# Kernel optimization log

Measured on AMD Instinct MI355X. Metric: run time of the kernel, lower is better.

## Reference

```python
import jax, jax.numpy as jnp
import numpy as np


def setup_inputs() -> dict:
    key = jax.random.key(0)
    kq, kk, kv = jax.random.split(key, 3)
    B, Q, K, D = 8, 2048, 2048, 1024
    return {
        "queries": jax.random.normal(kq, (B, Q, D), dtype=jnp.float32),
        "keys": jax.random.normal(kk, (B, K, D), dtype=jnp.float32),
        "values": jax.random.normal(kv, (B, K, D), dtype=jnp.float32),
    }


def reference(queries, keys, values):
    # scores: [B, Q, K] = queries @ keys^T
    scores = jnp.einsum("bqd,bkd->bqk", queries, keys)
    # NOTE: softmax over dim=1, i.e. the QUERY axis (non-standard)
    attn = jax.nn.softmax(scores, axis=1)
    # output: [B, Q, D]
    return jnp.einsum("bqk,bkd->bqd", attn, values)
```

## Files before the change

kernel.cpp:

```cpp
#include <hip/hip_runtime.h>
#include <stdint.h>

typedef _Float16 half8 __attribute__((ext_vector_type(8)));
typedef __attribute__((ext_vector_type(4))) float f32x4;
typedef __attribute__((ext_vector_type(8))) unsigned short us8;

__device__ inline unsigned short f2h(float x) {
  _Float16 h = (_Float16)x;
  return __builtin_bit_cast(unsigned short, h);
}

__device__ inline void ld16(const unsigned short* g, unsigned short* l) {
  __builtin_amdgcn_global_load_lds(
      (const __attribute__((address_space(1))) unsigned int*)g,
      (__attribute__((address_space(3))) unsigned int*)l, 16, 0, 0);
}

__global__ void k_cast16(const float* __restrict__ in, unsigned short* __restrict__ o, long n8) {
  long i = (long)blockIdx.x * blockDim.x + threadIdx.x;
  if (i >= n8) return;
  float4 a = ((const float4*)in)[i * 2];
  float4 b = ((const float4*)in)[i * 2 + 1];
  us8 h;
  h[0] = f2h(a.x); h[1] = f2h(a.y); h[2] = f2h(a.z); h[3] = f2h(a.w);
  h[4] = f2h(b.x); h[5] = f2h(b.y); h[6] = f2h(b.z); h[7] = f2h(b.w);
  *(us8*)(o + i * 8) = h;
}

__global__ void k_cast16c(const float* __restrict__ in, unsigned short* __restrict__ o,
                          int Kn, int Dn, int k0c, int Kc) {
  const long i = (long)blockIdx.x * blockDim.x + threadIdx.x;
  const long cols8 = (long)Kc * Dn / 8;
  const int b = (int)(i / cols8);
  const long j = i - (long)b * cols8;
  const float* p = in + (long)b * Kn * Dn + (long)k0c * Dn + j * 8;
  float4 a = *(const float4*)p;
  float4 c = *(const float4*)(p + 4);
  us8 h;
  h[0] = f2h(a.x); h[1] = f2h(a.y); h[2] = f2h(a.z); h[3] = f2h(a.w);
  h[4] = f2h(c.x); h[5] = f2h(c.y); h[6] = f2h(c.z); h[7] = f2h(c.w);
  *(us8*)(o + (long)b * Kc * Dn + j * 8) = h;
}

__global__ void k_transpose16(const float* __restrict__ V, unsigned short* __restrict__ VT,
                              int Kn, int Dn, int k0c, int Kc) {
  __shared__ unsigned short t[64][65];
  const int b = blockIdx.z;
  const int k0 = blockIdx.x * 64, d0 = blockIdx.y * 64;
  const int c = threadIdx.x & 63, rr = threadIdx.x >> 6;
  const float* pV = V + (long)b * Kn * Dn;
  unsigned short* pT = VT + (long)b * Dn * Kc;
#pragma unroll
  for (int i = 0; i < 16; ++i) {
    int r = rr + i * 4;
    t[r][c] = f2h(pV[(long)(k0c + k0 + r) * Dn + d0 + c]);
  }
  __syncthreads();
#pragma unroll
  for (int i = 0; i < 16; ++i) {
    int r = rr + i * 4;
    pT[(long)(d0 + r) * Kc + k0 + c] = t[c][r];
  }
}


#define SBAR() __builtin_amdgcn_s_barrier()
#define SCHED0() __builtin_amdgcn_sched_barrier(0)
#define VMC(n) do { asm volatile("s_waitcnt vmcnt(" #n ")" ::: "memory"); } while (0)

template <int STATS, int ACC>
__launch_bounds__(512, 2)
__global__ void k_gemm_bt(const unsigned short* __restrict__ A,
                          const unsigned short* __restrict__ B,
                          float* __restrict__ C, float2* __restrict__ ps,
                          int N, int Kin, long sA, long sB, long sC) {
  __shared__ unsigned short sAb[4][256 * 32];
  __shared__ unsigned short sBb[4][256 * 32];

  const int tid = threadIdx.x;
  const int lane = tid & 63, wave = tid >> 6;
  const int wr = wave >> 2, wc = wave & 3;
  const int l15 = lane & 15;

  const int nx = gridDim.x, ny = gridDim.y;
  int wg = ((int)blockIdx.z * ny + blockIdx.y) * nx + blockIdx.x;
  const int nwg = nx * ny * (int)gridDim.z;
  wg = (wg & 7) * (nwg >> 3) + (wg >> 3);
  const int tn = wg % nx, tm = (wg / nx) % ny, b = wg / (nx * ny);

  const unsigned short* pA = A + b * sA + (long)tm * 256 * Kin;
  const unsigned short* pB = B + b * sB + (long)tn * 256 * Kin;
  float* pC = C + b * sC;

  const int rlo = tid >> 2;
  const int csw = ((tid & 3) * 8) ^ (((rlo >> 1) & 3) << 3);
  const long ga = (long)rlo * Kin + csw;
  const long gh = (long)128 * Kin;

  const int ksw = ((lane >> 4) * 8) ^ (((l15 >> 1) & 3) << 3);
  const int aoff = (wr * 128 + l15) * 32 + ksw;
  const int boff = (wc * 64 + l15) * 32 + ksw;

#define STG(t, q) do { \
    ld16(pA + ga + (long)(t) * 32, &sAb[q][tid * 8]); \
    ld16(pA + ga + gh + (long)(t) * 32, &sAb[q][4096 + tid * 8]); \
    ld16(pB + ga + (long)(t) * 32, &sBb[q][tid * 8]); \
    ld16(pB + ga + gh + (long)(t) * 32, &sBb[q][4096 + tid * 8]); } while (0)

#define LDA8(q, m) (*(const half8*)&sAb[q][aoff + (m) * 512])
#define LDB8(q, n) (*(const half8*)&sBb[q][boff + (n) * 512])

  f32x4 acc[8][4];
#pragma unroll
  for (int i = 0; i < 8; ++i)
#pragma unroll
    for (int j = 0; j < 4; ++j)
#pragma unroll
      for (int r = 0; r < 4; ++r) acc[i][j][r] = 0.f;

  half8 aL[2][4], bC[2][4], aH[4];

#define READ_LO(s, q) \
  aL[s][0] = LDA8(q, 0); aL[s][1] = LDA8(q, 1); aL[s][2] = LDA8(q, 2); aL[s][3] = LDA8(q, 3); \
  bC[s][0] = LDB8(q, 0); bC[s][1] = LDB8(q, 1); bC[s][2] = LDB8(q, 2); bC[s][3] = LDB8(q, 3);

#define READ_HI(q) \
  aH[0] = LDA8(q, 4); aH[1] = LDA8(q, 5); aH[2] = LDA8(q, 6); aH[3] = LDA8(q, 7);

#define MFMA_ROW(m, a, s) \
  acc[m][0] = __builtin_amdgcn_mfma_f32_16x16x32_f16(a, bC[s][0], acc[m][0], 0, 0, 0); \
  acc[m][1] = __builtin_amdgcn_mfma_f32_16x16x32_f16(a, bC[s][1], acc[m][1], 0, 0, 0); \
  acc[m][2] = __builtin_amdgcn_mfma_f32_16x16x32_f16(a, bC[s][2], acc[m][2], 0, 0, 0); \
  acc[m][3] = __builtin_amdgcn_mfma_f32_16x16x32_f16(a, bC[s][3], acc[m][3], 0, 0, 0);

#define MFMA_LO(s) \
  __builtin_amdgcn_s_setprio(1); \
  MFMA_ROW(0, aL[s][0], s) MFMA_ROW(1, aL[s][1], s) \
  MFMA_ROW(2, aL[s][2], s) MFMA_ROW(3, aL[s][3], s) \
  __builtin_amdgcn_s_setprio(0);

#define MFMA_HI(s) \
  __builtin_amdgcn_s_setprio(1); \
  MFMA_ROW(4, aH[0], s) MFMA_ROW(5, aH[1], s) \
  MFMA_ROW(6, aH[2], s) MFMA_ROW(7, aH[3], s) \
  __builtin_amdgcn_s_setprio(0);

#define TILE_MAIN(t, s, sn) \
  READ_HI((t) & 3); \
  STG((t) + 2, ((t) + 2) & 3); \
  MFMA_LO(s) \
  VMC(4); SBAR(); SCHED0(); \
  READ_LO(sn, ((t) + 1) & 3); \
  MFMA_HI(s)

  const int nt = Kin >> 5;

  STG(0, 0);
  STG(1, 1);
  VMC(4); SBAR(); SCHED0();
  READ_LO(0, 0);

  for (int t = 0; t + 3 < nt; t += 2) {
    TILE_MAIN(t, 0, 1);
    TILE_MAIN(t + 1, 1, 0);
  }
  {
    READ_HI((nt - 2) & 3);
    MFMA_LO(0)
    VMC(0); SBAR(); SCHED0();
    READ_LO(1, (nt - 1) & 3);
    MFMA_HI(0)
    READ_HI((nt - 1) & 3);
    MFMA_LO(1)
    MFMA_HI(1)
  }

  const int crow0 = tm * 256 + wr * 128 + (lane >> 4) * 4;
  const int ccol0 = tn * 256 + wc * 64 + l15;
#pragma unroll
  for (int m = 0; m < 8; ++m)
#pragma unroll
    for (int n = 0; n < 4; ++n)
#pragma unroll
      for (int r = 0; r < 4; ++r) {
        long idx = (long)(crow0 + m * 16 + r) * N + ccol0 + n * 16;
        if constexpr (ACC) pC[idx] += acc[m][n][r];
        else pC[idx] = acc[m][n][r];
      }

  if constexpr (STATS) {
#pragma unroll
    for (int n = 0; n < 4; ++n) {
      float mx = -3.0e38f;
#pragma unroll
      for (int m = 0; m < 8; ++m)
#pragma unroll
        for (int r = 0; r < 4; ++r) mx = fmaxf(mx, acc[m][n][r]);
      mx = fmaxf(mx, __shfl_xor(mx, 16, 64));
      mx = fmaxf(mx, __shfl_xor(mx, 32, 64));
      float l = 0.f;
#pragma unroll
      for (int m = 0; m < 8; ++m)
#pragma unroll
        for (int r = 0; r < 4; ++r) l += __expf(acc[m][n][r] - mx);
      l += __shfl_xor(l, 16, 64);
      l += __shfl_xor(l, 32, 64);
      if (lane < 16) {
        int col = tn * 256 + wc * 64 + n * 16 + lane;
        ps[((long)(b * 16 + tm * 2 + wr)) * N + col] = make_float2(mx, l);
      }
    }
  }
}

__global__ void k_stats_combine(const float2* __restrict__ ps, float2* __restrict__ st, int Kc) {
  const long i = (long)blockIdx.x * blockDim.x + threadIdx.x;
  const int b = (int)(i / Kc), k = (int)(i % Kc);
  float M = -3.0e38f;
#pragma unroll
  for (int j = 0; j < 16; ++j) M = fmaxf(M, ps[((long)(b * 16 + j)) * Kc + k].x);
  float L = 0.f;
#pragma unroll
  for (int j = 0; j < 16; ++j) {
    float2 v = ps[((long)(b * 16 + j)) * Kc + k];
    L += v.y * __expf(v.x - M);
  }
  st[i] = make_float2(M, 1.0f / L);
}

__global__ void k_pcomp(const float* __restrict__ S, const float2* __restrict__ st,
                        unsigned short* __restrict__ P, int Kc) {
  const long i = (long)blockIdx.x * blockDim.x + threadIdx.x;
  const int kw = Kc >> 3;
  const long r = i / kw;
  const int kb = (int)(i - r * kw) * 8;
  const int b = (int)(r >> 11);
  const float* sp = S + r * Kc + kb;
  float4 s0 = *(const float4*)sp;
  float4 s1 = *(const float4*)(sp + 4);
  const float2* tp = st + (long)b * Kc + kb;
  us8 o;
  float sv[8] = {s0.x, s0.y, s0.z, s0.w, s1.x, s1.y, s1.z, s1.w};
#pragma unroll
  for (int j = 0; j < 8; ++j) {
    float2 t = tp[j];
    o[j] = f2h(__expf(sv[j] - t.x) * t.y);
  }
  *(us8*)(P + r * Kc + kb) = o;
}

extern "C" void kernel_launch(void* const* d_in, const int* in_sizes, int n_in,
                              void* d_out, int out_size, void* d_ws, size_t ws_size,
                              hipStream_t stream) {
  const float* Q = (const float*)d_in[0];
  const float* Kp = (const float*)d_in[1];
  const float* V = (const float*)d_in[2];
  float* out = (float*)d_out;

  constexpr int Bb = 8, Qn = 2048, Kn = 2048, Dn = 1024;
  constexpr long QD = (long)Qn * Dn;

  long Kc = 1024;
  for (;;) {
    size_t uKP = (size_t)Bb * Qn * Kc * 2;
    size_t need = (size_t)Bb * QD * 2
                + uKP
                + (size_t)Bb * Dn * Kc * 2
                + (size_t)Bb * Qn * Kc * 4
                + (size_t)Bb * 16 * Kc * 8
                + (size_t)Bb * Kc * 8;
    if (need <= ws_size || Kc == 256) break;
    Kc >>= 1;
  }
  const int nc = Kn / (int)Kc;

  char* w = (char*)d_ws;
  unsigned short* q16 = (unsigned short*)w; w += (size_t)Bb * QD * 2;
  unsigned short* kp  = (unsigned short*)w; w += (size_t)Bb * Qn * Kc * 2;
  unsigned short* vt  = (unsigned short*)w; w += (size_t)Bb * Dn * Kc * 2;
  float* S            = (float*)w;          w += (size_t)Bb * Qn * Kc * 4;
  float2* ps          = (float2*)w;         w += (size_t)Bb * 16 * Kc * 8;
  float2* st          = (float2*)w;

  unsigned short* k16c = kp;
  unsigned short* P    = kp;

  k_cast16<<<(int)(Bb * QD / 8 / 256), 256, 0, stream>>>(Q, q16, Bb * QD / 8);

  for (int c = 0; c < nc; ++c) {
    const int k0c = c * (int)Kc;
    k_cast16c<<<(int)((long)Bb * Kc * Dn / 8 / 256), 256, 0, stream>>>(
        Kp, k16c, Kn, Dn, k0c, (int)Kc);
    k_transpose16<<<dim3((int)Kc / 64, Dn / 64, Bb), 256, 0, stream>>>(
        V, vt, Kn, Dn, k0c, (int)Kc);
    k_gemm_bt<1, 0><<<dim3((int)Kc / 256, Qn / 256, Bb), 512, 0, stream>>>(
        q16, k16c, S, ps, (int)Kc, Dn, QD, (long)Kc * Dn, (long)Qn * Kc);
    k_stats_combine<<<Bb * (int)Kc / 256, 256, 0, stream>>>(ps, st, (int)Kc);
    k_pcomp<<<(int)((long)Bb * Qn * (Kc / 8) / 256), 256, 0, stream>>>(
        S, st, P, (int)Kc);
    if (c == 0)
      k_gemm_bt<0, 0><<<dim3(Dn / 256, Qn / 256, Bb), 512, 0, stream>>>(
          P, vt, out, nullptr, Dn, (int)Kc, (long)Qn * Kc, (long)Dn * Kc, QD);
    else
      k_gemm_bt<0, 1><<<dim3(Dn / 256, Qn / 256, Bb), 512, 0, stream>>>(
          P, vt, out, nullptr, Dn, (int)Kc, (long)Qn * Kc, (long)Dn * Kc, QD);
  }
}
```

Baseline: 454.5 us.

## Restructure GEMM main loop into 64-wide K groups with phased barriers

Replaces the 4-slot, 32-wide K pipeline with a double-buffered 64-wide K tile split into two halves. Each half is processed in phases that load fragments, issue one async global-to-LDS stage, wait on LDS, then run 16 MFMAs between barriers. The aim is a finer interleave of LDS reads, global loads and MFMA work in the style of the published 8-wave ping-pong schedule, with fewer fragment registers held at once. In exchange it adds many more barriers and lgkmcnt(0) waits per tile, which can serialize waves and stall the MFMA stream.

```diff
diff --git a/kernel.cpp b/kernel.cpp
--- a/kernel.cpp
+++ b/kernel.cpp
@@ -66,6 +66,7 @@
 
 #define SBAR() __builtin_amdgcn_s_barrier()
 #define SCHED0() __builtin_amdgcn_sched_barrier(0)
+#define LGKM0() do { asm volatile("s_waitcnt lgkmcnt(0)" ::: "memory"); SCHED0(); } while (0)
 #define VMC(n) do { asm volatile("s_waitcnt vmcnt(" #n ")" ::: "memory"); } while (0)
 
 template <int STATS, int ACC>
@@ -73,9 +74,9 @@
 __global__ void k_gemm_bt(const unsigned short* __restrict__ A,
                           const unsigned short* __restrict__ B,
                           float* __restrict__ C, float2* __restrict__ ps,
-                          int N, int Kin, long sA, long sB, long sC) {
-  __shared__ unsigned short sAb[4][256 * 32];
-  __shared__ unsigned short sBb[4][256 * 32];
+                          int N, int Kin, long sA_, long sB_, long sC_) {
+  __shared__ unsigned short sA[2][2][256 * 32];
+  __shared__ unsigned short sB[2][2][256 * 32];
 
   const int tid = threadIdx.x;
   const int lane = tid & 63, wave = tid >> 6;
@@ -88,27 +89,22 @@
   wg = (wg & 7) * (nwg >> 3) + (wg >> 3);
   const int tn = wg % nx, tm = (wg / nx) % ny, b = wg / (nx * ny);
 
-  const unsigned short* pA = A + b * sA + (long)tm * 256 * Kin;
-  const unsigned short* pB = B + b * sB + (long)tn * 256 * Kin;
-  float* pC = C + b * sC;
-
-  const int rlo = tid >> 2;
-  const int csw = ((tid & 3) * 8) ^ (((rlo >> 1) & 3) << 3);
-  const long ga = (long)rlo * Kin + csw;
-  const long gh = (long)128 * Kin;
-
-  const int ksw = ((lane >> 4) * 8) ^ (((l15 >> 1) & 3) << 3);
-  const int aoff = (wr * 128 + l15) * 32 + ksw;
-  const int boff = (wc * 64 + l15) * 32 + ksw;
-
-#define STG(t, q) do { \
-    ld16(pA + ga + (long)(t) * 32, &sAb[q][tid * 8]); \
-    ld16(pA + ga + gh + (long)(t) * 32, &sAb[q][4096 + tid * 8]); \
-    ld16(pB + ga + (long)(t) * 32, &sBb[q][tid * 8]); \
-    ld16(pB + ga + gh + (long)(t) * 32, &sBb[q][4096 + tid * 8]); } while (0)
-
-#define LDA8(q, m) (*(const half8*)&sAb[q][aoff + (m) * 512])
-#define LDB8(q, n) (*(const half8*)&sBb[q][boff + (n) * 512])
+  const unsigned short* pA = A + b * sA_ + (long)tm * 256 * Kin;
+  const unsigned short* pB = B + b * sB_ + (long)tn * 256 * Kin;
+  float* pC = C + b * sC_;
+
+  const int r1 = tid >> 2;
+  const int cswz = ((tid & 3) ^ ((r1 >> 1) & 3)) << 3;
+#define STAGE(Xp, Xs, kh, t) do { \
+    ld16(Xp + (long)r1 * Kin + (long)(t) * 64 + (kh) * 32 + cswz, \
+         &Xs[(t) & 1][kh][tid * 8]); \
+    ld16(Xp + (long)(r1 + 128) * Kin + (long)(t) * 64 + (kh) * 32 + cswz, \
+         &Xs[(t) & 1][kh][4096 + tid * 8]); \
+  } while (0)
+
+  const int cxl = (((lane >> 4) ^ ((l15 >> 1) & 3)) << 3);
+#define FA(d, kh, m) (*(const half8*)&sA[d][kh][(wr * 128 + (m) * 16 + l15) * 32 + cxl])
+#define FB(d, kh, n) (*(const half8*)&sB[d][kh][(wc * 64 + (n) * 16 + l15) * 32 + cxl])
 
   f32x4 acc[8][4];
 #pragma unroll
@@ -118,61 +114,64 @@
 #pragma unroll
       for (int r = 0; r < 4; ++r) acc[i][j][r] = 0.f;
 
-  half8 aL[2][4], bC[2][4], aH[4];
-
-#define READ_LO(s, q) \
-  aL[s][0] = LDA8(q, 0); aL[s][1] = LDA8(q, 1); aL[s][2] = LDA8(q, 2); aL[s][3] = LDA8(q, 3); \
-  bC[s][0] = LDB8(q, 0); bC[s][1] = LDB8(q, 1); bC[s][2] = LDB8(q, 2); bC[s][3] = LDB8(q, 3);
-
-#define READ_HI(q) \
-  aH[0] = LDA8(q, 4); aH[1] = LDA8(q, 5); aH[2] = LDA8(q, 6); aH[3] = LDA8(q, 7);
-
-#define MFMA_ROW(m, a, s) \
-  acc[m][0] = __builtin_amdgcn_mfma_f32_16x16x32_f16(a, bC[s][0], acc[m][0], 0, 0, 0); \
-  acc[m][1] = __builtin_amdgcn_mfma_f32_16x16x32_f16(a, bC[s][1], acc[m][1], 0, 0, 0); \
-  acc[m][2] = __builtin_amdgcn_mfma_f32_16x16x32_f16(a, bC[s][2], acc[m][2], 0, 0, 0); \
-  acc[m][3] = __builtin_amdgcn_mfma_f32_16x16x32_f16(a, bC[s][3], acc[m][3], 0, 0, 0);
-
-#define MFMA_LO(s) \
+  half8 aF[4], bF[4];
+
+#define PH_AB(d, kh) \
+  aF[0] = FA(d, kh, 0); aF[1] = FA(d, kh, 1); aF[2] = FA(d, kh, 2); aF[3] = FA(d, kh, 3); \
+  bF[0] = FB(d, kh, 0); bF[1] = FB(d, kh, 1); bF[2] = FB(d, kh, 2); bF[3] = FB(d, kh, 3);
+#define PH_A(d, kh) \
+  aF[0] = FA(d, kh, 4); aF[1] = FA(d, kh, 5); aF[2] = FA(d, kh, 6); aF[3] = FA(d, kh, 7);
+
+#define MM(mb) \
   __builtin_amdgcn_s_setprio(1); \
-  MFMA_ROW(0, aL[s][0], s) MFMA_ROW(1, aL[s][1], s) \
-  MFMA_ROW(2, aL[s][2], s) MFMA_ROW(3, aL[s][3], s) \
+  acc[mb+0][0] = __builtin_amdgcn_mfma_f32_16x16x32_f16(aF[0], bF[0], acc[mb+0][0], 0, 0, 0); \
+  acc[mb+0][1] = __builtin_amdgcn_mfma_f32_16x16x32_f16(aF[0], bF[1], acc[mb+0][1], 0, 0, 0); \
+  acc[mb+0][2] = __builtin_amdgcn_mfma_f32_16x16x32_f16(aF[0], bF[2], acc[mb+0][2], 0, 0, 0); \
+  acc[mb+0][3] = __builtin_amdgcn_mfma_f32_16x16x32_f16(aF[0], bF[3], acc[mb+0][3], 0, 0, 0); \
+  acc[mb+1][0] = __builtin_amdgcn_mfma_f32_16x16x32_f16(aF[1], bF[0], acc[mb+1][0], 0, 0, 0); \
+  acc[mb+1][1] = __builtin_amdgcn_mfma_f32_16x16x32_f16(aF[1], bF[1], acc[mb+1][1], 0, 0, 0); \
+  acc[mb+1][2] = __builtin_amdgcn_mfma_f32_16x16x32_f16(aF[1], bF[2], acc[mb+1][2], 0, 0, 0); \
+  acc[mb+1][3] = __builtin_amdgcn_mfma_f32_16x16x32_f16(aF[1], bF[3], acc[mb+1][3], 0, 0, 0); \
+  acc[mb+2][0] = __builtin_amdgcn_mfma_f32_16x16x32_f16(aF[2], bF[0], acc[mb+2][0], 0, 0, 0); \
+  acc[mb+2][1] = __builtin_amdgcn_mfma_f32_16x16x32_f16(aF[2], bF[1], acc[mb+2][1], 0, 0, 0); \
+  acc[mb+2][2] = __builtin_amdgcn_mfma_f32_16x16x32_f16(aF[2], bF[2], acc[mb+2][2], 0, 0, 0); \
+  acc[mb+2][3] = __builtin_amdgcn_mfma_f32_16x16x32_f16(aF[2], bF[3], acc[mb+2][3], 0, 0, 0); \
+  acc[mb+3][0] = __builtin_amdgcn_mfma_f32_16x16x32_f16(aF[3], bF[0], acc[mb+3][0], 0, 0, 0); \
+  acc[mb+3][1] = __builtin_amdgcn_mfma_f32_16x16x32_f16(aF[3], bF[1], acc[mb+3][1], 0, 0, 0); \
+  acc[mb+3][2] = __builtin_amdgcn_mfma_f32_16x16x32_f16(aF[3], bF[2], acc[mb+3][2], 0, 0, 0); \
+  acc[mb+3][3] = __builtin_amdgcn_mfma_f32_16x16x32_f16(aF[3], bF[3], acc[mb+3][3], 0, 0, 0); \
   __builtin_amdgcn_s_setprio(0);
 
-#define MFMA_HI(s) \
-  __builtin_amdgcn_s_setprio(1); \
-  MFMA_ROW(4, aH[0], s) MFMA_ROW(5, aH[1], s) \
-  MFMA_ROW(6, aH[2], s) MFMA_ROW(7, aH[3], s) \
-  __builtin_amdgcn_s_setprio(0);
-
-#define TILE_MAIN(t, s, sn) \
-  READ_HI((t) & 3); \
-  STG((t) + 2, ((t) + 2) & 3); \
-  MFMA_LO(s) \
-  VMC(4); SBAR(); SCHED0(); \
-  READ_LO(sn, ((t) + 1) & 3); \
-  MFMA_HI(s)
-
-  const int nt = Kin >> 5;
-
-  STG(0, 0);
-  STG(1, 1);
-  VMC(4); SBAR(); SCHED0();
-  READ_LO(0, 0);
-
-  for (int t = 0; t + 3 < nt; t += 2) {
-    TILE_MAIN(t, 0, 1);
-    TILE_MAIN(t + 1, 1, 0);
-  }
+#define GROUP_FULL(t) do { \
+    const int d_ = (t) & 1; \
+    PH_AB(d_, 0); STAGE(pA, sA, 1, (t) + 1); SBAR(); LGKM0(); MM(0) SBAR(); \
+    PH_A(d_, 0);  STAGE(pB, sB, 1, (t) + 1); SBAR(); LGKM0(); MM(4) VMC(6); SBAR(); \
+    PH_AB(d_, 1); STAGE(pA, sA, 0, (t) + 2); SBAR(); LGKM0(); MM(0) SBAR(); \
+    PH_A(d_, 1);  STAGE(pB, sB, 0, (t) + 2); SBAR(); LGKM0(); MM(4) VMC(6); SBAR(); \
+  } while (0)
+
+  const int nt = Kin >> 6;
+
+  STAGE(pA, sA, 0, 0); STAGE(pB, sB, 0, 0);
+  STAGE(pA, sA, 1, 0); STAGE(pB, sB, 1, 0);
+  STAGE(pA, sA, 0, 1); STAGE(pB, sB, 0, 1);
+  VMC(8); SBAR();
+
+  for (int t = 0; t + 2 < nt; ++t) GROUP_FULL(t);
+
   {
-    READ_HI((nt - 2) & 3);
-    MFMA_LO(0)
-    VMC(0); SBAR(); SCHED0();
-    READ_LO(1, (nt - 1) & 3);
-    MFMA_HI(0)
-    READ_HI((nt - 1) & 3);
-    MFMA_LO(1)
-    MFMA_HI(1)
+    const int d_ = (nt - 2) & 1;
+    PH_AB(d_, 0); STAGE(pA, sA, 1, nt - 1); SBAR(); LGKM0(); MM(0) SBAR();
+    PH_A(d_, 0);  STAGE(pB, sB, 1, nt - 1); SBAR(); LGKM0(); MM(4) VMC(6); SBAR();
+    PH_AB(d_, 1);                           SBAR(); LGKM0(); MM(0) SBAR();
+    PH_A(d_, 1);                            SBAR(); LGKM0(); MM(4) VMC(4); SBAR();
+  }
+  {
+    const int d_ = (nt - 1) & 1;
+    PH_AB(d_, 0); SBAR(); LGKM0(); MM(0) SBAR();
+    PH_A(d_, 0);  SBAR(); LGKM0(); MM(4) VMC(0); SBAR();
+    PH_AB(d_, 1); SBAR(); LGKM0(); MM(0) SBAR();
+    PH_A(d_, 1);  SBAR(); LGKM0(); MM(4)
   }
 
   const int crow0 = tm * 256 + wr * 128 + (lane >> 4) * 4;
```

Result: no change. 460.5 us (+1.3%).
